# Kernel tuning notes

Hardware: AMD Instinct MI355X
Metric: run time of the kernel (lower is better)

Reference implementation:

```python
import jax, jax.numpy as jnp
import numpy as np

EPS = 1e-12


def setup_inputs() -> dict:
    key = jax.random.key(0)
    k = jax.random.split(key, 6)
    B, C, T, A = 8, 1536, 4096, 128
    x = jax.random.normal(k[0], (B, C, T), dtype=jnp.float32)
    lengths = jax.random.randint(k[1], (B,), T // 2, T + 1, dtype=jnp.int64)
    W1 = jax.random.normal(k[2], (A, 3 * C), dtype=jnp.float32) * (1.0 / np.sqrt(3 * C))
    b1 = jax.random.normal(k[3], (A,), dtype=jnp.float32) * 0.01
    W2 = jax.random.normal(k[4], (1, A), dtype=jnp.float32) * (1.0 / np.sqrt(A))
    b2 = jax.random.normal(k[5], (1,), dtype=jnp.float32) * 0.01
    return {"x": x, "lengths": lengths, "W1": W1, "b1": b1, "W2": W2, "b2": b2}


def reference(x, lengths, W1, b1, W2, b2):
    # x: [B, C, T]
    B, C, T = x.shape
    mask = (jnp.arange(T)[None, :] < lengths[:, None]).astype(x.dtype)  # [B, T]
    m3 = mask[:, None, :]  # [B, 1, T]

    # causal (cumulative) mean / std for global context
    count = jnp.clip(jnp.cumsum(mask, axis=1), 1.0)[:, None, :]        # [B, 1, T]
    causal_mean = jnp.cumsum(x * m3, axis=2) / count                   # [B, C, T]
    causal_var = jnp.cumsum(x * x * m3, axis=2) / count - causal_mean ** 2
    causal_std = jnp.sqrt(jnp.clip(causal_var, EPS))

    attn_in = jnp.concatenate([x, causal_mean, causal_std], axis=1)    # [B, 3C, T]
    attn_in = attn_in.transpose(0, 2, 1)                               # [B, T, 3C]

    h = jnp.tanh(attn_in @ W1.T + b1)                                  # [B, T, A]
    logits = (h @ W2.T + b2)[..., 0]                                   # [B, T]

    # logits are query-independent, so causal softmax row q is
    # exp(l_k) / cumsum(exp(l))_q for k <= q -> O(T*C) prefix scan.
    e = jnp.exp(logits - jnp.max(logits, axis=1, keepdims=True))       # [B, T]
    Z = jnp.cumsum(e, axis=1)[:, None, :]                              # [B, 1, T]
    ew = e[:, None, :]                                                 # [B, 1, T]

    weighted_mean = jnp.cumsum(ew * x, axis=2) / Z                     # [B, C, T]
    sq_diff = (x - weighted_mean) ** 2
    weighted_var = jnp.cumsum(ew * sq_diff, axis=2) / Z
    weighted_std = jnp.sqrt(jnp.clip(weighted_var, EPS))

    # each causal softmax row sums to 1 -> final weights are 1/(T+eps)
    fw = 1.0 / (jnp.asarray(T, x.dtype) + EPS)
    final_mean = jnp.sum(weighted_mean, axis=2) * fw                   # [B, C]
    final_std = jnp.sum(weighted_std, axis=2) * fw
    return jnp.concatenate([final_mean, final_std], axis=1)            # [B, 2C]
```

## Files before the change

kernel.cpp:

```cpp
#include <hip/hip_runtime.h>
#include <hip/hip_bf16.h>

#define B_ 8
#define C_ 1536
#define T_ 4096
#define A_ 128
#define K3_ 4608
#define M32_ 128
#define SCW_ 104

typedef _Float16 h8  __attribute__((ext_vector_type(8)));
typedef float    f4  __attribute__((ext_vector_type(4)));

__global__ void k0_pack(const float* __restrict__ W1, _Float16* __restrict__ W1f) {
    int i = blockIdx.x * 256 + threadIdx.x;
    if (i >= A_ * K3_) return;
    int a = i / K3_, k = i - a * K3_;
    int t8 = a >> 4, r15 = a & 15;
    int kb = k >> 5, q = (k >> 3) & 3, j = k & 7;
    int lane = q * 16 + r15;
    W1f[(size_t)((kb * 8 + t8) * 64 + lane) * 8 + j] = (_Float16)W1[i];
}

__global__ __launch_bounds__(256) void k1_carryT(
    const float* __restrict__ x, const int* __restrict__ lens,
    float2* __restrict__ carryT)
{
    const int rowid = blockIdx.x * 4 + (threadIdx.x >> 6);
    const int lane  = threadIdx.x & 63;
    const int b     = rowid / C_;
    const int c     = rowid - b * C_;
    const int len   = lens[b];
    const float* xr = x + (size_t)rowid * T_;
    float2* ct = carryT + (size_t)b * M32_ * C_ + c;
    const int grp = lane >> 3;
    float base1 = 0.f, base2 = 0.f;
#pragma unroll
    for (int g = 0; g < 16; ++g) {
        const int t0g = g * 256;
        if (t0g >= len) {
            if ((lane & 7) == 0) ct[(size_t)(g * 8 + grp) * C_] = make_float2(base1, base2);
            continue;
        }
        float4 v = *(const float4*)(xr + t0g + lane * 4);
        float s1, s2;
        if (t0g + 256 <= len) {
            s1 = v.x + v.y + v.z + v.w;
            s2 = v.x * v.x + v.y * v.y + v.z * v.z + v.w * v.w;
        } else {
            const int tb = t0g + lane * 4;
            float vs[4] = {v.x, v.y, v.z, v.w};
            s1 = 0.f; s2 = 0.f;
#pragma unroll
            for (int j = 0; j < 4; ++j) {
                float m = (tb + j < len) ? vs[j] : 0.f;
                s1 += m; s2 += m * vs[j];
            }
        }
        float g1 = s1, g2 = s2;
        g1 += __shfl_xor(g1, 1, 64); g2 += __shfl_xor(g2, 1, 64);
        g1 += __shfl_xor(g1, 2, 64); g2 += __shfl_xor(g2, 2, 64);
        g1 += __shfl_xor(g1, 4, 64); g2 += __shfl_xor(g2, 4, 64);
        float V1 = g1, V2 = g2;
#pragma unroll
        for (int d = 8; d < 64; d <<= 1) {
            float o1 = __shfl_up(V1, d, 64);
            float o2 = __shfl_up(V2, d, 64);
            if (lane >= d) { V1 += o1; V2 += o2; }
        }
        const float e1 = V1 - g1, e2 = V2 - g2;
        if ((lane & 7) == 0)
            ct[(size_t)(g * 8 + grp) * C_] = make_float2(base1 + e1, base2 + e2);
        base1 += __shfl(V1, 63, 64);
        base2 += __shfl(V2, 63, 64);
    }
}

__global__ __launch_bounds__(256, 3) void k2g(
    const float* __restrict__ x, const int* __restrict__ lens,
    const float2* __restrict__ carryT, const _Float16* __restrict__ W1f,
    const float* __restrict__ b1, const float* __restrict__ W2,
    float* __restrict__ logits)
{
    __shared__ __align__(16) char smem[32768];
    __shared__ float s_b1[A_], s_w2[A_];

    const int tid = threadIdx.x, lane = tid & 63, w = tid >> 6;
    const int bid = blockIdx.x;
    const int b   = bid >> 7;
    const int m   = bid & 127;
    const int t0  = m << 5;
    const int len = lens[b];
    if (tid < A_) { s_b1[tid] = b1[tid]; s_w2[tid] = W2[tid]; }

    const int kc = lane >> 1;
    const int th = lane & 1;
    const int c_base = w * 384;
    _Float16* sc = (_Float16*)smem + w * (32 * SCW_);
    const h8* W1f8 = (const h8*)W1f;
    const bool full = (t0 + 32) <= len;
    const int tb = t0 + th * 16;

    f4 acc[2][8] = {};

    const float* xptr = x + ((size_t)b * C_ + c_base + kc) * T_ + tb;

    for (int step = 0; step < 12; ++step) {
        float xs[16];
        *(float4*)&xs[0]  = ((const float4*)xptr)[0];
        *(float4*)&xs[4]  = ((const float4*)xptr)[1];
        *(float4*)&xs[8]  = ((const float4*)xptr)[2];
        *(float4*)&xs[12] = ((const float4*)xptr)[3];
        xptr += 32 * (size_t)T_;
        const float2 cr =
            carryT[((size_t)b * M32_ + m) * C_ + c_base + step * 32 + kc];

        float ls1 = 0.f, ls2 = 0.f;
        if (full) {
#pragma unroll
            for (int j = 0; j < 16; ++j) { ls1 += xs[j]; ls2 += xs[j] * xs[j]; }
        } else {
#pragma unroll
            for (int j = 0; j < 16; ++j) {
                float mv = (tb + j < len) ? xs[j] : 0.f;
                ls1 += mv; ls2 += mv * xs[j];
            }
        }
        const float o1 = __shfl_xor(ls1, 1, 64);
        const float o2 = __shfl_xor(ls2, 1, 64);
        float r1 = cr.x + (th ? o1 : 0.f);
        float r2 = cr.y + (th ? o2 : 0.f);
#pragma unroll
        for (int j = 0; j < 16; ++j) {
            const float xval = xs[j];
            const float mv = (full || (tb + j < len)) ? xval : 0.f;
            r1 += mv; r2 += mv * xval;
            const float rn = __builtin_amdgcn_rcpf((float)min(tb + j + 1, len));
            const float mn = r1 * rn;
            const float var = r2 * rn - mn * mn;
            const float sd = sqrtf(fmaxf(var, 1e-12f));
            const int row = th * 16 + j;
            sc[row * SCW_ + kc]      = (_Float16)xval;
            sc[row * SCW_ + 32 + kc] = (_Float16)mn;
            sc[row * SCW_ + 64 + kc] = (_Float16)sd;
        }
        const int t15 = lane & 15, k8 = lane >> 4;
        const int kbS = w * 12 + step;
#pragma unroll
        for (int p = 0; p < 3; ++p) {
            h8 bf0 = *(const h8*)&sc[t15 * SCW_ + p * 32 + k8 * 8];
            h8 bf1 = *(const h8*)&sc[(16 + t15) * SCW_ + p * 32 + k8 * 8];
            const int kb = p * 48 + kbS;
#pragma unroll
            for (int ii = 0; ii < 8; ++ii) {
                h8 af = W1f8[(size_t)(kb * 8 + ii) * 64 + lane];
                acc[0][ii] = __builtin_amdgcn_mfma_f32_16x16x32_f16(af, bf0, acc[0][ii], 0, 0, 0);
                acc[1][ii] = __builtin_amdgcn_mfma_f32_16x16x32_f16(af, bf1, acc[1][ii], 0, 0, 0);
            }
        }
    }

    __syncthreads();
    float* red = (float*)smem;
    if (w >= 2) {
        float* r = red + (size_t)(w - 2) * 4096;
#pragma unroll
        for (int nn = 0; nn < 2; ++nn)
#pragma unroll
            for (int ii = 0; ii < 8; ++ii)
#pragma unroll
                for (int rg = 0; rg < 4; ++rg)
                    r[(nn * 32 + ii * 4 + rg) * 64 + lane] = acc[nn][ii][rg];
    }
    __syncthreads();
    if (w < 2) {
        float* r = red + (size_t)w * 4096;
#pragma unroll
        for (int nn = 0; nn < 2; ++nn)
#pragma unroll
            for (int ii = 0; ii < 8; ++ii)
#pragma unroll
                for (int rg = 0; rg < 4; ++rg)
                    acc[nn][ii][rg] += r[(nn * 32 + ii * 4 + rg) * 64 + lane];
    }
    __syncthreads();
    if (w == 1) {
#pragma unroll
        for (int nn = 0; nn < 2; ++nn)
#pragma unroll
            for (int ii = 0; ii < 8; ++ii)
#pragma unroll
                for (int rg = 0; rg < 4; ++rg)
                    red[(nn * 32 + ii * 4 + rg) * 64 + lane] = acc[nn][ii][rg];
    }
    __syncthreads();
    if (w == 0) {
        const int q = lane >> 4;
#pragma unroll
        for (int nn = 0; nn < 2; ++nn) {
            float pr = 0.f;
#pragma unroll
            for (int ii = 0; ii < 8; ++ii)
#pragma unroll
                for (int rg = 0; rg < 4; ++rg) {
                    float v = acc[nn][ii][rg] + red[(nn * 32 + ii * 4 + rg) * 64 + lane];
                    int a = ii * 16 + q * 4 + rg;
                    pr += tanhf(v + s_b1[a]) * s_w2[a];
                }
            pr += __shfl_xor(pr, 16, 64);
            pr += __shfl_xor(pr, 32, 64);
            if (lane < 16)
                logits[(size_t)b * T_ + t0 + nn * 16 + lane] = pr;
        }
    }
}

__global__ __launch_bounds__(1024) void k3_softmax(
    const float* __restrict__ logits, float* __restrict__ earr,
    float* __restrict__ zarr)
{
    __shared__ float wsum[16];
    const int b = blockIdx.x, tid = threadIdx.x, lane = tid & 63, w = tid >> 6;
    float4 v = *(const float4*)(logits + (size_t)b * T_ + tid * 4);
    float e0 = expf(v.x), e1 = expf(v.y), e2 = expf(v.z), e3 = expf(v.w);
    float s = (e0 + e1) + (e2 + e3);
    float V = s;
#pragma unroll
    for (int d = 1; d < 64; d <<= 1) {
        float o = __shfl_up(V, d, 64);
        if (lane >= d) V += o;
    }
    if (lane == 63) wsum[w] = V;
    __syncthreads();
    float wb = 0.f;
#pragma unroll
    for (int i = 0; i < 16; ++i) wb += (i < w) ? wsum[i] : 0.f;
    float run = wb + (V - s);
    float4 ev, zv;
    ev.x = e0; run += e0; zv.x = run;
    ev.y = e1; run += e1; zv.y = run;
    ev.z = e2; run += e2; zv.z = run;
    ev.w = e3; run += e3; zv.w = run;
    *(float4*)(earr + (size_t)b * T_ + tid * 4) = ev;
    *(float4*)(zarr + (size_t)b * T_ + tid * 4) = zv;
}

__global__ __launch_bounds__(256) void k4_wstats(
    const float* __restrict__ x, const float* __restrict__ earr,
    const float* __restrict__ zarr, float* __restrict__ out)
{
    const int rowid = blockIdx.x * 4 + (threadIdx.x >> 6);
    const int lane  = threadIdx.x & 63;
    const int b = rowid / C_;
    const int c = rowid - b * C_;
    const float* xr = x + (size_t)rowid * T_;
    const float* er = earr + (size_t)b * T_;
    const float* zr = zarr + (size_t)b * T_;
    float am = 0.f, asd = 0.f;
    float baseS = 0.f, baseD = 0.f;
#pragma unroll
    for (int g = 0; g < 16; ++g) {
        const int off = g * 256 + lane * 4;
        float4 xv = *(const float4*)(xr + off);
        float4 ev = *(const float4*)(er + off);
        float4 zv = *(const float4*)(zr + off);
        float s0 = ev.x * xv.x;
        float s1 = s0 + ev.y * xv.y;
        float s2 = s1 + ev.z * xv.z;
        float s3 = s2 + ev.w * xv.w;
        float V = s3;
#pragma unroll
        for (int d = 1; d < 64; d <<= 1) {
            float o = __shfl_up(V, d, 64);
            if (lane >= d) V += o;
        }
        const float Sx = baseS + (V - s3);
        baseS += __shfl(V, 63, 64);
        const float rz0 = __builtin_amdgcn_rcpf(zv.x);
        const float rz1 = __builtin_amdgcn_rcpf(zv.y);
        const float rz2 = __builtin_amdgcn_rcpf(zv.z);
        const float rz3 = __builtin_amdgcn_rcpf(zv.w);
        const float wm0 = (Sx + s0) * rz0;
        const float wm1 = (Sx + s1) * rz1;
        const float wm2 = (Sx + s2) * rz2;
        const float wm3 = (Sx + s3) * rz3;
        am += (wm0 + wm1) + (wm2 + wm3);
        const float d0 = xv.x - wm0;
        const float d1 = xv.y - wm1;
        const float d2 = xv.z - wm2;
        const float d3 = xv.w - wm3;
        float q0 = ev.x * d0 * d0;
        float q1 = q0 + ev.y * d1 * d1;
        float q2 = q1 + ev.z * d2 * d2;
        float q3 = q2 + ev.w * d3 * d3;
        float W = q3;
#pragma unroll
        for (int d = 1; d < 64; d <<= 1) {
            float o = __shfl_up(W, d, 64);
            if (lane >= d) W += o;
        }
        const float Dx = baseD + (W - q3);
        baseD += __shfl(W, 63, 64);
        const float v0 = (Dx + q0) * rz0;
        const float v1 = (Dx + q1) * rz1;
        const float v2 = (Dx + q2) * rz2;
        const float v3 = (Dx + q3) * rz3;
        asd += (sqrtf(fmaxf(v0, 1e-12f)) + sqrtf(fmaxf(v1, 1e-12f)))
             + (sqrtf(fmaxf(v2, 1e-12f)) + sqrtf(fmaxf(v3, 1e-12f)));
    }
#pragma unroll
    for (int d = 1; d < 64; d <<= 1) {
        am  += __shfl_xor(am, d, 64);
        asd += __shfl_xor(asd, d, 64);
    }
    if (lane == 0) {
        out[(size_t)b * (2 * C_) + c]      = am  * (1.f / 4096.f);
        out[(size_t)b * (2 * C_) + C_ + c] = asd * (1.f / 4096.f);
    }
}

extern "C" void kernel_launch(void* const* d_in, const int* in_sizes, int n_in,
                              void* d_out, int out_size, void* d_ws, size_t ws_size,
                              hipStream_t stream) {
    const float* x    = (const float*)d_in[0];
    const int*   lens = (const int*)d_in[1];
    const float* W1   = (const float*)d_in[2];
    const float* b1   = (const float*)d_in[3];
    const float* W2   = (const float*)d_in[4];
    float* out = (float*)d_out;
    char* ws = (char*)d_ws;

    float2*    carryT = (float2*)ws;
    _Float16*  W1f    = (_Float16*)(ws + 12582912);
    float*     logits = (float*)(ws + 13762560);
    float*     earr   = (float*)(ws + 13893632);
    float*     zarr   = (float*)(ws + 14024704);

    k0_pack   <<<(A_ * K3_ + 255) / 256, 256, 0, stream>>>(W1, W1f);
    k1_carryT <<<(B_ * C_) / 4, 256, 0, stream>>>(x, lens, carryT);
    k2g       <<<B_ * M32_, 256, 0, stream>>>(x, lens, carryT, W1f, b1, W2, logits);
    k3_softmax<<<B_, 1024, 0, stream>>>(logits, earr, zarr);
    k4_wstats <<<(B_ * C_) / 4, 256, 0, stream>>>(x, earr, zarr, out);
}
```

Before: 481.0 us.

## Retile projection GEMM to per-wave 16-step tiles and pair channel rows in scans

The projection kernel now gives each wave its own 16-timestep tile covering the full K range, over 48 steps. This removes the cross-wave LDS reduction and its syncthreads, and raises the occupancy target. It also adds an XOR-swizzled LDS layout, hoisted reciprocals and a fast path for padded timesteps. The carry kernel now emits prefix sums at 16-step granularity and processes two channels per wave, and the weighted-stats kernel also handles two channel rows per wave to reuse the e/Z loads. The trade-offs are a carry workspace twice as large and W1 fragments re-read by every wave instead of being shared across waves.

```diff
diff --git a/kernel.cpp b/kernel.cpp
--- a/kernel.cpp
+++ b/kernel.cpp
@@ -6,7 +6,7 @@
 #define T_ 4096
 #define A_ 128
 #define K3_ 4608
-#define M32_ 128
+#define M16_ 256
 #define SCW_ 104
 
 typedef _Float16 h8  __attribute__((ext_vector_type(8)));
@@ -26,193 +26,198 @@
     const float* __restrict__ x, const int* __restrict__ lens,
     float2* __restrict__ carryT)
 {
-    const int rowid = blockIdx.x * 4 + (threadIdx.x >> 6);
-    const int lane  = threadIdx.x & 63;
-    const int b     = rowid / C_;
-    const int c     = rowid - b * C_;
-    const int len   = lens[b];
-    const float* xr = x + (size_t)rowid * T_;
-    float2* ct = carryT + (size_t)b * M32_ * C_ + c;
-    const int grp = lane >> 3;
-    float base1 = 0.f, base2 = 0.f;
+    const int pid  = blockIdx.x * 4 + (threadIdx.x >> 6);
+    const int lane = threadIdx.x & 63;
+    const int b    = pid / 768;
+    const int c0   = (pid - b * 768) * 2;
+    const int len  = lens[b];
+    const float* xr0 = x + ((size_t)b * C_ + c0) * T_;
+    const float* xr1 = xr0 + T_;
+    float2* ct = carryT + (size_t)b * M16_ * C_ + c0;
+    const int grp = lane >> 2;
+    float bA1 = 0.f, bA2 = 0.f, bB1 = 0.f, bB2 = 0.f;
 #pragma unroll
     for (int g = 0; g < 16; ++g) {
         const int t0g = g * 256;
         if (t0g >= len) {
-            if ((lane & 7) == 0) ct[(size_t)(g * 8 + grp) * C_] = make_float2(base1, base2);
+            if ((lane & 3) == 0) {
+                float4 st = {bA1, bA2, bB1, bB2};
+                *(float4*)&ct[(size_t)(g * 16 + grp) * C_] = st;
+            }
             continue;
         }
-        float4 v = *(const float4*)(xr + t0g + lane * 4);
-        float s1, s2;
+        float4 va = *(const float4*)(xr0 + t0g + lane * 4);
+        float4 vb = *(const float4*)(xr1 + t0g + lane * 4);
+        float sA1, sA2, sB1, sB2;
         if (t0g + 256 <= len) {
-            s1 = v.x + v.y + v.z + v.w;
-            s2 = v.x * v.x + v.y * v.y + v.z * v.z + v.w * v.w;
+            sA1 = (va.x + va.y) + (va.z + va.w);
+            sA2 = (va.x * va.x + va.y * va.y) + (va.z * va.z + va.w * va.w);
+            sB1 = (vb.x + vb.y) + (vb.z + vb.w);
+            sB2 = (vb.x * vb.x + vb.y * vb.y) + (vb.z * vb.z + vb.w * vb.w);
         } else {
-            const int tb = t0g + lane * 4;
-            float vs[4] = {v.x, v.y, v.z, v.w};
-            s1 = 0.f; s2 = 0.f;
+            const int tbase = t0g + lane * 4;
+            float av[4] = {va.x, va.y, va.z, va.w};
+            float bv[4] = {vb.x, vb.y, vb.z, vb.w};
+            sA1 = sA2 = sB1 = sB2 = 0.f;
 #pragma unroll
             for (int j = 0; j < 4; ++j) {
-                float m = (tb + j < len) ? vs[j] : 0.f;
-                s1 += m; s2 += m * vs[j];
-            }
-        }
-        float g1 = s1, g2 = s2;
-        g1 += __shfl_xor(g1, 1, 64); g2 += __shfl_xor(g2, 1, 64);
-        g1 += __shfl_xor(g1, 2, 64); g2 += __shfl_xor(g2, 2, 64);
-        g1 += __shfl_xor(g1, 4, 64); g2 += __shfl_xor(g2, 4, 64);
-        float V1 = g1, V2 = g2;
-#pragma unroll
-        for (int d = 8; d < 64; d <<= 1) {
-            float o1 = __shfl_up(V1, d, 64);
-            float o2 = __shfl_up(V2, d, 64);
-            if (lane >= d) { V1 += o1; V2 += o2; }
-        }
-        const float e1 = V1 - g1, e2 = V2 - g2;
-        if ((lane & 7) == 0)
-            ct[(size_t)(g * 8 + grp) * C_] = make_float2(base1 + e1, base2 + e2);
-        base1 += __shfl(V1, 63, 64);
-        base2 += __shfl(V2, 63, 64);
-    }
-}
-
-__global__ __launch_bounds__(256, 3) void k2g(
+                bool in = (tbase + j) < len;
+                float ma = in ? av[j] : 0.f;
+                float mb = in ? bv[j] : 0.f;
+                sA1 += ma; sA2 += ma * av[j];
+                sB1 += mb; sB2 += mb * bv[j];
+            }
+        }
+        sA1 += __shfl_xor(sA1, 1, 64); sA2 += __shfl_xor(sA2, 1, 64);
+        sB1 += __shfl_xor(sB1, 1, 64); sB2 += __shfl_xor(sB2, 1, 64);
+        sA1 += __shfl_xor(sA1, 2, 64); sA2 += __shfl_xor(sA2, 2, 64);
+        sB1 += __shfl_xor(sB1, 2, 64); sB2 += __shfl_xor(sB2, 2, 64);
+        float VA1 = sA1, VA2 = sA2, VB1 = sB1, VB2 = sB2;
+#pragma unroll
+        for (int d = 4; d < 64; d <<= 1) {
+            float oA1 = __shfl_up(VA1, d, 64);
+            float oA2 = __shfl_up(VA2, d, 64);
+            float oB1 = __shfl_up(VB1, d, 64);
+            float oB2 = __shfl_up(VB2, d, 64);
+            if (lane >= d) { VA1 += oA1; VA2 += oA2; VB1 += oB1; VB2 += oB2; }
+        }
+        if ((lane & 3) == 0) {
+            float4 st = {bA1 + VA1 - sA1, bA2 + VA2 - sA2,
+                         bB1 + VB1 - sB1, bB2 + VB2 - sB2};
+            *(float4*)&ct[(size_t)(g * 16 + grp) * C_] = st;
+        }
+        bA1 += __shfl(VA1, 63, 64);
+        bA2 += __shfl(VA2, 63, 64);
+        bB1 += __shfl(VB1, 63, 64);
+        bB2 += __shfl(VB2, 63, 64);
+    }
+}
+
+__global__ __launch_bounds__(256, 4) void k2h(
     const float* __restrict__ x, const int* __restrict__ lens,
     const float2* __restrict__ carryT, const _Float16* __restrict__ W1f,
     const float* __restrict__ b1, const float* __restrict__ W2,
     float* __restrict__ logits)
 {
-    __shared__ __align__(16) char smem[32768];
+    __shared__ _Float16 sc_all[4 * 16 * SCW_];
     __shared__ float s_b1[A_], s_w2[A_];
 
     const int tid = threadIdx.x, lane = tid & 63, w = tid >> 6;
     const int bid = blockIdx.x;
-    const int b   = bid >> 7;
-    const int m   = bid & 127;
-    const int t0  = m << 5;
+    const int b   = bid >> 6;
+    const int t0w = (bid & 63) * 64 + w * 16;
+    const int m16 = t0w >> 4;
     const int len = lens[b];
     if (tid < A_) { s_b1[tid] = b1[tid]; s_w2[tid] = W2[tid]; }
+    __syncthreads();
 
     const int kc = lane >> 1;
     const int th = lane & 1;
-    const int c_base = w * 384;
-    _Float16* sc = (_Float16*)smem + w * (32 * SCW_);
+    const int tb = t0w + th * 8;
+    _Float16* sc = sc_all + w * (16 * SCW_);
+    const int kcol = (((kc >> 3) ^ (th << 1)) << 3) + (kc & 7);
+    _Float16* scw = sc + th * 8 * SCW_ + kcol;
     const h8* W1f8 = (const h8*)W1f;
-    const bool full = (t0 + 32) <= len;
-    const int tb = t0 + th * 16;
-
-    f4 acc[2][8] = {};
-
-    const float* xptr = x + ((size_t)b * C_ + c_base + kc) * T_ + tb;
-
-    for (int step = 0; step < 12; ++step) {
-        float xs[16];
-        *(float4*)&xs[0]  = ((const float4*)xptr)[0];
-        *(float4*)&xs[4]  = ((const float4*)xptr)[1];
-        *(float4*)&xs[8]  = ((const float4*)xptr)[2];
-        *(float4*)&xs[12] = ((const float4*)xptr)[3];
+
+    const bool beyond = t0w >= len;
+    const bool full   = (t0w + 16) <= len;
+
+    float rn_l[8];
+#pragma unroll
+    for (int j = 0; j < 8; ++j)
+        rn_l[j] = __builtin_amdgcn_rcpf((float)min(tb + j + 1, len));
+
+    f4 acc[8] = {};
+    const float* xptr = x + ((size_t)b * C_ + kc) * T_ + tb;
+    const float2* crp = carryT + ((size_t)b * M16_ + m16) * C_ + kc;
+
+    const int t15 = lane & 15, k8 = lane >> 4;
+    const int rdbase = t15 * SCW_ + ((k8 ^ ((t15 >> 3) << 1)) << 3);
+
+    for (int step = 0; step < 48; ++step) {
+        float4 xa = ((const float4*)xptr)[0];
+        float4 xb = ((const float4*)xptr)[1];
         xptr += 32 * (size_t)T_;
-        const float2 cr =
-            carryT[((size_t)b * M32_ + m) * C_ + c_base + step * 32 + kc];
-
-        float ls1 = 0.f, ls2 = 0.f;
-        if (full) {
-#pragma unroll
-            for (int j = 0; j < 16; ++j) { ls1 += xs[j]; ls2 += xs[j] * xs[j]; }
+        const float2 cr = crp[(size_t)step * 32];
+        float xs[8] = {xa.x, xa.y, xa.z, xa.w, xb.x, xb.y, xb.z, xb.w};
+
+        if (beyond) {
+            const float rn0 = rn_l[0];
+            const float mn = cr.x * rn0;
+            const float sd = sqrtf(fmaxf(cr.y * rn0 - mn * mn, 1e-12f));
+            const _Float16 hm = (_Float16)mn, hs = (_Float16)sd;
+#pragma unroll
+            for (int j = 0; j < 8; ++j) {
+                scw[j * SCW_]      = (_Float16)xs[j];
+                scw[j * SCW_ + 32] = hm;
+                scw[j * SCW_ + 64] = hs;
+            }
         } else {
-#pragma unroll
-            for (int j = 0; j < 16; ++j) {
-                float mv = (tb + j < len) ? xs[j] : 0.f;
-                ls1 += mv; ls2 += mv * xs[j];
-            }
-        }
-        const float o1 = __shfl_xor(ls1, 1, 64);
-        const float o2 = __shfl_xor(ls2, 1, 64);
-        float r1 = cr.x + (th ? o1 : 0.f);
-        float r2 = cr.y + (th ? o2 : 0.f);
-#pragma unroll
-        for (int j = 0; j < 16; ++j) {
-            const float xval = xs[j];
-            const float mv = (full || (tb + j < len)) ? xval : 0.f;
-            r1 += mv; r2 += mv * xval;
-            const float rn = __builtin_amdgcn_rcpf((float)min(tb + j + 1, len));
-            const float mn = r1 * rn;
-            const float var = r2 * rn - mn * mn;
-            const float sd = sqrtf(fmaxf(var, 1e-12f));
-            const int row = th * 16 + j;
-            sc[row * SCW_ + kc]      = (_Float16)xval;
-            sc[row * SCW_ + 32 + kc] = (_Float16)mn;
-            sc[row * SCW_ + 64 + kc] = (_Float16)sd;
-        }
-        const int t15 = lane & 15, k8 = lane >> 4;
-        const int kbS = w * 12 + step;
+            float ls1 = 0.f, ls2 = 0.f;
+            if (full) {
+#pragma unroll
+                for (int j = 0; j < 8; ++j) { ls1 += xs[j]; ls2 += xs[j] * xs[j]; }
+            } else {
+#pragma unroll
+                for (int j = 0; j < 8; ++j) {
+                    float mv = (tb + j < len) ? xs[j] : 0.f;
+                    ls1 += mv; ls2 += mv * xs[j];
+                }
+            }
+            const float o1 = __shfl_xor(ls1, 1, 64);
+            const float o2 = __shfl_xor(ls2, 1, 64);
+            float r1 = cr.x + (th ? o1 : 0.f);
+            float r2 = cr.y + (th ? o2 : 0.f);
+            if (full) {
+#pragma unroll
+                for (int j = 0; j < 8; ++j) {
+                    const float xval = xs[j];
+                    r1 += xval; r2 += xval * xval;
+                    const float mn = r1 * rn_l[j];
+                    const float sd = sqrtf(fmaxf(r2 * rn_l[j] - mn * mn, 1e-12f));
+                    scw[j * SCW_]      = (_Float16)xval;
+                    scw[j * SCW_ + 32] = (_Float16)mn;
+                    scw[j * SCW_ + 64] = (_Float16)sd;
+                }
+            } else {
+#pragma unroll
+                for (int j = 0; j < 8; ++j) {
+                    const float xval = xs[j];
+                    const float mv = (tb + j < len) ? xval : 0.f;
+                    r1 += mv; r2 += mv * xval;
+                    const float mn = r1 * rn_l[j];
+                    const float sd = sqrtf(fmaxf(r2 * rn_l[j] - mn * mn, 1e-12f));
+                    scw[j * SCW_]      = (_Float16)xval;
+                    scw[j * SCW_ + 32] = (_Float16)mn;
+                    scw[j * SCW_ + 64] = (_Float16)sd;
+                }
+            }
+        }
 #pragma unroll
         for (int p = 0; p < 3; ++p) {
-            h8 bf0 = *(const h8*)&sc[t15 * SCW_ + p * 32 + k8 * 8];
-            h8 bf1 = *(const h8*)&sc[(16 + t15) * SCW_ + p * 32 + k8 * 8];
-            const int kb = p * 48 + kbS;
+            h8 bf = *(const h8*)&sc[rdbase + p * 32];
+            const int kb = p * 48 + step;
 #pragma unroll
             for (int ii = 0; ii < 8; ++ii) {
                 h8 af = W1f8[(size_t)(kb * 8 + ii) * 64 + lane];
-                acc[0][ii] = __builtin_amdgcn_mfma_f32_16x16x32_f16(af, bf0, acc[0][ii], 0, 0, 0);
-                acc[1][ii] = __builtin_amdgcn_mfma_f32_16x16x32_f16(af, bf1, acc[1][ii], 0, 0, 0);
-            }
-        }
-    }
-
-    __syncthreads();
-    float* red = (float*)smem;
-    if (w >= 2) {
-        float* r = red + (size_t)(w - 2) * 4096;
-#pragma unroll
-        for (int nn = 0; nn < 2; ++nn)
-#pragma unroll
-            for (int ii = 0; ii < 8; ++ii)
-#pragma unroll
-                for (int rg = 0; rg < 4; ++rg)
-                    r[(nn * 32 + ii * 4 + rg) * 64 + lane] = acc[nn][ii][rg];
-    }
-    __syncthreads();
-    if (w < 2) {
-        float* r = red + (size_t)w * 4096;
-#pragma unroll
-        for (int nn = 0; nn < 2; ++nn)
-#pragma unroll
-            for (int ii = 0; ii < 8; ++ii)
-#pragma unroll
-                for (int rg = 0; rg < 4; ++rg)
-                    acc[nn][ii][rg] += r[(nn * 32 + ii * 4 + rg) * 64 + lane];
-    }
-    __syncthreads();
-    if (w == 1) {
-#pragma unroll
-        for (int nn = 0; nn < 2; ++nn)
-#pragma unroll
-            for (int ii = 0; ii < 8; ++ii)
-#pragma unroll
-                for (int rg = 0; rg < 4; ++rg)
-                    red[(nn * 32 + ii * 4 + rg) * 64 + lane] = acc[nn][ii][rg];
-    }
-    __syncthreads();
-    if (w == 0) {
-        const int q = lane >> 4;
-#pragma unroll
-        for (int nn = 0; nn < 2; ++nn) {
-            float pr = 0.f;
-#pragma unroll
-            for (int ii = 0; ii < 8; ++ii)
-#pragma unroll
-                for (int rg = 0; rg < 4; ++rg) {
-                    float v = acc[nn][ii][rg] + red[(nn * 32 + ii * 4 + rg) * 64 + lane];
-                    int a = ii * 16 + q * 4 + rg;
-                    pr += tanhf(v + s_b1[a]) * s_w2[a];
-                }
-            pr += __shfl_xor(pr, 16, 64);
-            pr += __shfl_xor(pr, 32, 64);
-            if (lane < 16)
-                logits[(size_t)b * T_ + t0 + nn * 16 + lane] = pr;
-        }
-    }
+                acc[ii] = __builtin_amdgcn_mfma_f32_16x16x32_f16(af, bf, acc[ii], 0, 0, 0);
+            }
+        }
+    }
+
+    const int q = lane >> 4;
+    float pr = 0.f;
+#pragma unroll
+    for (int ii = 0; ii < 8; ++ii)
+#pragma unroll
+        for (int rg = 0; rg < 4; ++rg) {
+            const int a = ii * 16 + q * 4 + rg;
+            pr += tanhf(acc[ii][rg] + s_b1[a]) * s_w2[a];
+        }
+    pr += __shfl_xor(pr, 16, 64);
+    pr += __shfl_xor(pr, 32, 64);
+    if (lane < 16)
+        logits[(size_t)b * T_ + t0w + t15] = pr;
 }
 
 __global__ __launch_bounds__(1024) void k3_softmax(
@@ -249,73 +254,96 @@
     const float* __restrict__ x, const float* __restrict__ earr,
     const float* __restrict__ zarr, float* __restrict__ out)
 {
-    const int rowid = blockIdx.x * 4 + (threadIdx.x >> 6);
-    const int lane  = threadIdx.x & 63;
-    const int b = rowid / C_;
-    const int c = rowid - b * C_;
-    const float* xr = x + (size_t)rowid * T_;
+    const int pid  = blockIdx.x * 4 + (threadIdx.x >> 6);
+    const int lane = threadIdx.x & 63;
+    const int b = pid / 768;
+    const int c = (pid - b * 768) * 2;
+    const float* xr0 = x + ((size_t)b * C_ + c) * T_;
+    const float* xr1 = xr0 + T_;
     const float* er = earr + (size_t)b * T_;
     const float* zr = zarr + (size_t)b * T_;
-    float am = 0.f, asd = 0.f;
-    float baseS = 0.f, baseD = 0.f;
-#pragma unroll
+    float am0 = 0.f, asd0 = 0.f, am1 = 0.f, asd1 = 0.f;
+    float bS0 = 0.f, bD0 = 0.f, bS1 = 0.f, bD1 = 0.f;
+#pragma unroll 4
     for (int g = 0; g < 16; ++g) {
         const int off = g * 256 + lane * 4;
-        float4 xv = *(const float4*)(xr + off);
         float4 ev = *(const float4*)(er + off);
         float4 zv = *(const float4*)(zr + off);
-        float s0 = ev.x * xv.x;
-        float s1 = s0 + ev.y * xv.y;
-        float s2 = s1 + ev.z * xv.z;
-        float s3 = s2 + ev.w * xv.w;
-        float V = s3;
+        float4 xa = *(const float4*)(xr0 + off);
+        float4 xb = *(const float4*)(xr1 + off);
+        float sA0 = ev.x * xa.x;
+        float sA1 = sA0 + ev.y * xa.y;
+        float sA2 = sA1 + ev.z * xa.z;
+        float sA3 = sA2 + ev.w * xa.w;
+        float sB0 = ev.x * xb.x;
+        float sB1 = sB0 + ev.y * xb.y;
+        float sB2 = sB1 + ev.z * xb.z;
+        float sB3 = sB2 + ev.w * xb.w;
+        float VA = sA3, VB = sB3;
 #pragma unroll
         for (int d = 1; d < 64; d <<= 1) {
-            float o = __shfl_up(V, d, 64);
-            if (lane >= d) V += o;
-        }
-        const float Sx = baseS + (V - s3);
-        baseS += __shfl(V, 63, 64);
+            float oA = __shfl_up(VA, d, 64);
+            float oB = __shfl_up(VB, d, 64);
+            if (lane >= d) { VA += oA; VB += oB; }
+        }
+        const float SxA = bS0 + (VA - sA3);
+        const float SxB = bS1 + (VB - sB3);
+        bS0 += __shfl(VA, 63, 64);
+        bS1 += __shfl(VB, 63, 64);
         const float rz0 = __builtin_amdgcn_rcpf(zv.x);
         const float rz1 = __builtin_amdgcn_rcpf(zv.y);
         const float rz2 = __builtin_amdgcn_rcpf(zv.z);
         const float rz3 = __builtin_amdgcn_rcpf(zv.w);
-        const float wm0 = (Sx + s0) * rz0;
-        const float wm1 = (Sx + s1) * rz1;
-        const float wm2 = (Sx + s2) * rz2;
-        const float wm3 = (Sx + s3) * rz3;
-        am += (wm0 + wm1) + (wm2 + wm3);
-        const float d0 = xv.x - wm0;
-        const float d1 = xv.y - wm1;
-        const float d2 = xv.z - wm2;
-        const float d3 = xv.w - wm3;
-        float q0 = ev.x * d0 * d0;
-        float q1 = q0 + ev.y * d1 * d1;
-        float q2 = q1 + ev.z * d2 * d2;
-        float q3 = q2 + ev.w * d3 * d3;
-        float W = q3;
+        const float wmA0 = (SxA + sA0) * rz0, wmA1 = (SxA + sA1) * rz1;
+        const float wmA2 = (SxA + sA2) * rz2, wmA3 = (SxA + sA3) * rz3;
+        const float wmB0 = (SxB + sB0) * rz0, wmB1 = (SxB + sB1) * rz1;
+        const float wmB2 = (SxB + sB2) * rz2, wmB3 = (SxB + sB3) * rz3;
+        am0 += (wmA0 + wmA1) + (wmA2 + wmA3);
+        am1 += (wmB0 + wmB1) + (wmB2 + wmB3);
+        const float dA0 = xa.x - wmA0, dA1 = xa.y - wmA1;
+        const float dA2 = xa.z - wmA2, dA3 = xa.w - wmA3;
+        const float dB0 = xb.x - wmB0, dB1 = xb.y - wmB1;
+        const float dB2 = xb.z - wmB2, dB3 = xb.w - wmB3;
+        float qA0 = ev.x * dA0 * dA0;
+        float qA1 = qA0 + ev.y * dA1 * dA1;
+        float qA2 = qA1 + ev.z * dA2 * dA2;
+        float qA3 = qA2 + ev.w * dA3 * dA3;
+        float qB0 = ev.x * dB0 * dB0;
+        float qB1 = qB0 + ev.y * dB1 * dB1;
+        float qB2 = qB1 + ev.z * dB2 * dB2;
+        float qB3 = qB2 + ev.w * dB3 * dB3;
+        float WA = qA3, WB = qB3;
 #pragma unroll
         for (int d = 1; d < 64; d <<= 1) {
-            float o = __shfl_up(W, d, 64);
-            if (lane >= d) W += o;
-        }
-        const float Dx = baseD + (W - q3);
-        baseD += __shfl(W, 63, 64);
-        const float v0 = (Dx + q0) * rz0;
-        const float v1 = (Dx + q1) * rz1;
-        const float v2 = (Dx + q2) * rz2;
-        const float v3 = (Dx + q3) * rz3;
-        asd += (sqrtf(fmaxf(v0, 1e-12f)) + sqrtf(fmaxf(v1, 1e-12f)))
-             + (sqrtf(fmaxf(v2, 1e-12f)) + sqrtf(fmaxf(v3, 1e-12f)));
+            float oA = __shfl_up(WA, d, 64);
+            float oB = __shfl_up(WB, d, 64);
+            if (lane >= d) { WA += oA; WB += oB; }
+        }
+        const float DxA = bD0 + (WA - qA3);
+        const float DxB = bD1 + (WB - qB3);
+        bD0 += __shfl(WA, 63, 64);
+        bD1 += __shfl(WB, 63, 64);
+        asd0 += (sqrtf(fmaxf((DxA + qA0) * rz0, 1e-12f)) +
+                 sqrtf(fmaxf((DxA + qA1) * rz1, 1e-12f))) +
+                (sqrtf(fmaxf((DxA + qA2) * rz2, 1e-12f)) +
+                 sqrtf(fmaxf((DxA + qA3) * rz3, 1e-12f)));
+        asd1 += (sqrtf(fmaxf((DxB + qB0) * rz0, 1e-12f)) +
+                 sqrtf(fmaxf((DxB + qB1) * rz1, 1e-12f))) +
+                (sqrtf(fmaxf((DxB + qB2) * rz2, 1e-12f)) +
+                 sqrtf(fmaxf((DxB + qB3) * rz3, 1e-12f)));
     }
 #pragma unroll
     for (int d = 1; d < 64; d <<= 1) {
-        am  += __shfl_xor(am, d, 64);
-        asd += __shfl_xor(asd, d, 64);
+        am0  += __shfl_xor(am0, d, 64);
+        am1  += __shfl_xor(am1, d, 64);
+        asd0 += __shfl_xor(asd0, d, 64);
+        asd1 += __shfl_xor(asd1, d, 64);
     }
     if (lane == 0) {
-        out[(size_t)b * (2 * C_) + c]      = am  * (1.f / 4096.f);
-        out[(size_t)b * (2 * C_) + C_ + c] = asd * (1.f / 4096.f);
+        out[(size_t)b * (2 * C_) + c]          = am0  * (1.f / 4096.f);
+        out[(size_t)b * (2 * C_) + c + 1]      = am1  * (1.f / 4096.f);
+        out[(size_t)b * (2 * C_) + C_ + c]     = asd0 * (1.f / 4096.f);
+        out[(size_t)b * (2 * C_) + C_ + c + 1] = asd1 * (1.f / 4096.f);
     }
 }
 
@@ -331,14 +359,14 @@
     char* ws = (char*)d_ws;
 
     float2*    carryT = (float2*)ws;
-    _Float16*  W1f    = (_Float16*)(ws + 12582912);
-    float*     logits = (float*)(ws + 13762560);
-    float*     earr   = (float*)(ws + 13893632);
-    float*     zarr   = (float*)(ws + 14024704);
+    _Float16*  W1f    = (_Float16*)(ws + 25165824);
+    float*     logits = (float*)(ws + 26345472);
+    float*     earr   = (float*)(ws + 26476544);
+    float*     zarr   = (float*)(ws + 26607616);
 
     k0_pack   <<<(A_ * K3_ + 255) / 256, 256, 0, stream>>>(W1, W1f);
-    k1_carryT <<<(B_ * C_) / 4, 256, 0, stream>>>(x, lens, carryT);
-    k2g       <<<B_ * M32_, 256, 0, stream>>>(x, lens, carryT, W1f, b1, W2, logits);
+    k1_carryT <<<(B_ * C_) / 8, 256, 0, stream>>>(x, lens, carryT);
+    k2h       <<<B_ * 64, 256, 0, stream>>>(x, lens, carryT, W1f, b1, W2, logits);
     k3_softmax<<<B_, 1024, 0, stream>>>(logits, earr, zarr);
-    k4_wstats <<<(B_ * C_) / 4, 256, 0, stream>>>(x, earr, zarr, out);
-}
+    k4_wstats <<<(B_ * C_) / 8, 256, 0, stream>>>(x, earr, zarr, out);
+}
```

After: 527.2 us. 9.6% more time.
